# Kernel tuning notes

Hardware: AMD Instinct MI355X
Metric: run time of the kernel (lower is better)

## Reference

```python
import jax, jax.numpy as jnp
import numpy as np

B, S, D = 2, 2048, 1024
H, HKV, HD = 16, 4, 64
FF = 4096
WINDOW = 1024
EPS = 1e-6


def _rope_tables(seq_len, head_dim, base=10000.0):
    inv_freq = 1.0 / (base ** (np.arange(0, head_dim, 2, dtype=np.float32) / head_dim))
    t = np.arange(seq_len, dtype=np.float32)
    freqs = np.outer(t, inv_freq)                       # [S, HD/2]
    emb = np.concatenate([freqs, freqs], axis=-1)       # [S, HD]
    return jnp.asarray(np.cos(emb)), jnp.asarray(np.sin(emb))


def setup_inputs() -> dict:
    key = jax.random.key(0)
    ks = jax.random.split(key, 16)
    s = lambda fan: 1.0 / np.sqrt(fan)
    cos, sin = _rope_tables(S, HD)
    return {
        "hidden_states": jax.random.normal(ks[0], (B, S, D), jnp.float32),
        "cos": cos, "sin": sin,
        "wq": jax.random.normal(ks[1], (D, H * HD), jnp.float32) * s(D),
        "bq": jnp.zeros((H * HD,), jnp.float32),
        "wk": jax.random.normal(ks[2], (D, HKV * HD), jnp.float32) * s(D),
        "bk": jnp.zeros((HKV * HD,), jnp.float32),
        "wv": jax.random.normal(ks[3], (D, HKV * HD), jnp.float32) * s(D),
        "bv": jnp.zeros((HKV * HD,), jnp.float32),
        "wo": jax.random.normal(ks[4], (H * HD, D), jnp.float32) * s(H * HD),
        "ln1_w": jnp.ones((D,), jnp.float32),
        "ln2_w": jnp.ones((D,), jnp.float32),
        "w_gate": jax.random.normal(ks[5], (D, FF), jnp.float32) * s(D),
        "w_up": jax.random.normal(ks[6], (D, FF), jnp.float32) * s(D),
        "w_down": jax.random.normal(ks[7], (FF, D), jnp.float32) * s(FF),
    }


def _rmsnorm(x, w, eps=EPS):
    var = jnp.mean(x.astype(jnp.float32) ** 2, axis=-1, keepdims=True)
    return (x * jax.lax.rsqrt(var + eps)).astype(x.dtype) * w


def _rotate_half(x):
    x1, x2 = jnp.split(x, 2, axis=-1)
    return jnp.concatenate([-x2, x1], axis=-1)


def reference(hidden_states, cos, sin, wq, bq, wk, bk, wv, bv, wo,
              ln1_w, ln2_w, w_gate, w_up, w_down):
    residual = hidden_states
    h = _rmsnorm(hidden_states, ln1_w)

    # projections -> [B, S, H, HD]
    q = (h @ wq + bq).reshape(B, S, H, HD)
    k = (h @ wk + bk).reshape(B, S, HKV, HD)
    v = (h @ wv + bv).reshape(B, S, HKV, HD)

    # RoPE
    c = cos[None, :, None, :]
    sn = sin[None, :, None, :]
    q = q * c + _rotate_half(q) * sn
    k = k * c + _rotate_half(k) * sn

    # GQA: repeat KV heads to H heads
    groups = H // HKV
    k = jnp.repeat(k, groups, axis=2)  # [B, S, H, HD]
    v = jnp.repeat(v, groups, axis=2)

    # sliding-window causal attention (flex_attention block-mask semantics)
    scale = 1.0 / np.sqrt(HD)
    scores = jnp.einsum("bqhd,bkhd->bhqk", q, k) * scale  # [B, H, S, S]
    i = jnp.arange(S)[:, None]
    j = jnp.arange(S)[None, :]
    mask = (j <= i) & (i - j < WINDOW)
    scores = jnp.where(mask[None, None], scores, jnp.finfo(scores.dtype).min)
    attn = jax.nn.softmax(scores, axis=-1)
    ctx = jnp.einsum("bhqk,bkhd->bqhd", attn, v).reshape(B, S, H * HD)

    h = residual + ctx @ wo

    residual2 = h
    h2 = _rmsnorm(h, ln2_w)
    mlp = (jax.nn.silu(h2 @ w_gate) * (h2 @ w_up)) @ w_down
    return residual2 + mlp
```

## Files before the change

### kernel.cpp

```cpp
#include <hip/hip_runtime.h>
#include <hip/hip_bf16.h>
#include <hip/hip_fp16.h>
#include <math.h>

#define BB 2
#define SS 2048
#define DD 1024
#define HH 16
#define HKVN 4
#define HDIM 64
#define FFD 4096
#define WND 1024
#define EPSF 1e-6f

typedef _Float16 f16;
typedef _Float16 half8 __attribute__((ext_vector_type(8)));
typedef float f32x4 __attribute__((ext_vector_type(4)));
typedef unsigned int u32;

#define GLOAD_LDS(gp, lp)                                                  \
  __builtin_amdgcn_global_load_lds(                                        \
      (const __attribute__((address_space(1))) u32*)(gp),                  \
      (__attribute__((address_space(3))) u32*)(lp), 16, 0, 0)

static __device__ inline u32 pack2(float a, float b) {
  unsigned short ua = __builtin_bit_cast(unsigned short, (f16)a);
  unsigned short ub = __builtin_bit_cast(unsigned short, (f16)b);
  return (u32)ua | ((u32)ub << 16);
}

__global__ __launch_bounds__(256) void transpose_cast_kernel(
    const float* __restrict__ W, f16* __restrict__ Wt, int K, int N) {
  __shared__ float tile[64][65];
  int k0 = blockIdx.y * 64, n0 = blockIdx.x * 64;
  int tx = threadIdx.x & 63, tr = threadIdx.x >> 6;
#pragma unroll
  for (int i = 0; i < 16; i++) {
    int r = tr + i * 4;
    tile[r][tx] = W[(size_t)(k0 + r) * N + n0 + tx];
  }
  __syncthreads();
#pragma unroll
  for (int i = 0; i < 16; i++) {
    int r = tr + i * 4;
    Wt[(size_t)(n0 + r) * K + k0 + tx] = (f16)tile[tx][r];
  }
}

__global__ __launch_bounds__(256) void biascat_kernel(
    const float* __restrict__ bq, const float* __restrict__ bk,
    const float* __restrict__ bv, float* __restrict__ o) {
  int i = blockIdx.x * 256 + threadIdx.x;
  if (i < 1024)
    o[i] = bq[i];
  else if (i < 1280)
    o[i] = bk[i - 1024];
  else if (i < 1536)
    o[i] = bv[i - 1280];
}

__global__ __launch_bounds__(256) void rmsnorm_kernel(
    const float* __restrict__ x, const float* __restrict__ w,
    f16* __restrict__ out, int d) {
  int row = blockIdx.x;
  const float* xr = x + (size_t)row * d;
  float ss = 0.f;
  for (int i = threadIdx.x; i < d; i += blockDim.x) {
    float v = xr[i];
    ss += v * v;
  }
  __shared__ float red[8];
  for (int o = 32; o > 0; o >>= 1) ss += __shfl_down(ss, o, 64);
  int wid = threadIdx.x >> 6, lane = threadIdx.x & 63;
  if (lane == 0) red[wid] = ss;
  __syncthreads();
  if (threadIdx.x == 0) {
    float t = 0.f;
    int nw = blockDim.x >> 6;
    for (int i = 0; i < nw; i++) t += red[i];
    red[0] = rsqrtf(t / (float)d + EPSF);
  }
  __syncthreads();
  float rs = red[0];
  f16* orow = out + (size_t)row * d;
  for (int i = threadIdx.x; i < d; i += blockDim.x) {
    orow[i] = (f16)(xr[i] * rs * w[i]);
  }
}

__global__ __launch_bounds__(256) void mfma_gemm(
    const f16* __restrict__ A, const f16* __restrict__ Bt,
    const float* __restrict__ bias, const float* __restrict__ resid,
    float* __restrict__ Cf, float* __restrict__ Cf2, int M, int N, int K,
    int KL) {
  __shared__ __align__(16) char smem[3 * 16384];
  const int tid = threadIdx.x;
  const int lane = tid & 63;
  const int wid = tid >> 6;
  const int wr = wid >> 1, wc = wid & 1;
  const int row0 = blockIdx.y * 128, col0 = blockIdx.x * 128;
  const int koff = blockIdx.z * KL;

  f32x4 acc[4][4];
#pragma unroll
  for (int m = 0; m < 4; m++)
#pragma unroll
    for (int n = 0; n < 4; n++) acc[m][n] = (f32x4){0.f, 0.f, 0.f, 0.f};

  auto stage = [&](int buf, int k0) {
    char* base = smem + buf * 16384;
#pragma unroll
    for (int q = 0; q < 2; q++) {
      int s = wid * 128 + q * 64 + lane;
      int r = s >> 2;
      int cg = (s & 3) ^ ((r >> 1) & 3);
      size_t goff = (size_t)r * K + k0 + cg * 8;
      u32 ldsb = (u32)((wid * 2 + q) * 1024);
      GLOAD_LDS(A + (size_t)row0 * K + goff, base + ldsb);
      GLOAD_LDS(Bt + (size_t)col0 * K + goff, base + 8192 + ldsb);
    }
  };
  auto off = [&](int r, int g) -> int {
    return r * 64 + ((g ^ ((r >> 1) & 3)) << 4);
  };

  const int nt = KL / 32;
  stage(0, koff);
  if (nt > 1) stage(1, koff + 32);
  int cur = 0;
  const int g = lane >> 4, l15 = lane & 15;
  for (int t = 0; t < nt; t++) {
    if (t + 1 < nt)
      asm volatile("s_waitcnt vmcnt(4)" ::: "memory");
    else
      asm volatile("s_waitcnt vmcnt(0)" ::: "memory");
    asm volatile("s_waitcnt lgkmcnt(0)" ::: "memory");
    __builtin_amdgcn_sched_barrier(0);
    __builtin_amdgcn_s_barrier();
    __builtin_amdgcn_sched_barrier(0);
    const char* base = smem + cur * 16384;
    half8 af[4], bf[4];
#pragma unroll
    for (int m = 0; m < 4; m++) {
      int r = wr * 64 + m * 16 + l15;
      af[m] = *(const half8*)(base + off(r, g));
    }
#pragma unroll
    for (int n = 0; n < 4; n++) {
      int c = wc * 64 + n * 16 + l15;
      bf[n] = *(const half8*)(base + 8192 + off(c, g));
    }
    if (t + 2 < nt) {
      int nb = cur + 2;
      if (nb >= 3) nb -= 3;
      stage(nb, koff + (t + 2) * 32);
    }
    __builtin_amdgcn_s_setprio(1);
#pragma unroll
    for (int m = 0; m < 4; m++)
#pragma unroll
      for (int n = 0; n < 4; n++)
        acc[m][n] =
            __builtin_amdgcn_mfma_f32_16x16x32_f16(af[m], bf[n], acc[m][n], 0, 0, 0);
    __builtin_amdgcn_s_setprio(0);
    cur = (cur + 1 == 3) ? 0 : cur + 1;
  }

  float* cw = (blockIdx.z == 0) ? Cf : Cf2;
#pragma unroll
  for (int m = 0; m < 4; m++) {
#pragma unroll
    for (int n = 0; n < 4; n++) {
#pragma unroll
      for (int v = 0; v < 4; v++) {
        int r = row0 + wr * 64 + m * 16 + (lane >> 4) * 4 + v;
        int c = col0 + wc * 64 + n * 16 + (lane & 15);
        float vv = acc[m][n][v];
        if (bias) vv += bias[c];
        if (resid) vv += resid[(size_t)r * N + c];
        cw[(size_t)r * N + c] = vv;
      }
    }
  }
}

__global__ __launch_bounds__(512) void gateup_gemm(
    const f16* __restrict__ A, const f16* __restrict__ Wg,
    const f16* __restrict__ Wu, f16* __restrict__ ACT, int M, int N, int K) {
  __shared__ __align__(16) char smem[3 * 24576];
  const int tid = threadIdx.x;
  const int lane = tid & 63;
  const int wid = tid >> 6;
  const int wr = wid >> 1;
  const int wc = wid & 1;
  const int row0 = blockIdx.y * 128, col0 = blockIdx.x * 128;

  f32x4 accg[2][4], accu[2][4];
#pragma unroll
  for (int m = 0; m < 2; m++)
#pragma unroll
    for (int n = 0; n < 4; n++) {
      accg[m][n] = (f32x4){0.f, 0.f, 0.f, 0.f};
      accu[m][n] = (f32x4){0.f, 0.f, 0.f, 0.f};
    }

  auto stage = [&](int buf, int k0) {
    char* base = smem + buf * 24576;
    int s = tid;
    int r = s >> 2;
    int cg = (s & 3) ^ ((r >> 1) & 3);
    size_t goff = (size_t)r * K + k0 + cg * 8;
    u32 ldsb = (u32)(wid * 1024);
    GLOAD_LDS(A + (size_t)row0 * K + goff, base + ldsb);
    GLOAD_LDS(Wg + (size_t)col0 * K + goff, base + 8192 + ldsb);
    GLOAD_LDS(Wu + (size_t)col0 * K + goff, base + 16384 + ldsb);
  };
  auto off = [&](int r, int g) -> int {
    return r * 64 + ((g ^ ((r >> 1) & 3)) << 4);
  };

  const int nt = K / 32;
  stage(0, 0);
  if (nt > 1) stage(1, 32);
  int cur = 0;
  const int g = lane >> 4, l15 = lane & 15;
  for (int t = 0; t < nt; t++) {
    if (t + 1 < nt)
      asm volatile("s_waitcnt vmcnt(3)" ::: "memory");
    else
      asm volatile("s_waitcnt vmcnt(0)" ::: "memory");
    asm volatile("s_waitcnt lgkmcnt(0)" ::: "memory");
    __builtin_amdgcn_sched_barrier(0);
    __builtin_amdgcn_s_barrier();
    __builtin_amdgcn_sched_barrier(0);
    const char* base = smem + cur * 24576;
    half8 af[2], gf[4], uf[4];
#pragma unroll
    for (int m = 0; m < 2; m++) {
      int r = wr * 32 + m * 16 + l15;
      af[m] = *(const half8*)(base + off(r, g));
    }
#pragma unroll
    for (int n = 0; n < 4; n++) {
      int c = wc * 64 + n * 16 + l15;
      gf[n] = *(const half8*)(base + 8192 + off(c, g));
      uf[n] = *(const half8*)(base + 16384 + off(c, g));
    }
    if (t + 2 < nt) {
      int nb = cur + 2;
      if (nb >= 3) nb -= 3;
      stage(nb, (t + 2) * 32);
    }
    __builtin_amdgcn_s_setprio(1);
#pragma unroll
    for (int m = 0; m < 2; m++)
#pragma unroll
      for (int n = 0; n < 4; n++) {
        accg[m][n] =
            __builtin_amdgcn_mfma_f32_16x16x32_f16(af[m], gf[n], accg[m][n], 0, 0, 0);
        accu[m][n] =
            __builtin_amdgcn_mfma_f32_16x16x32_f16(af[m], uf[n], accu[m][n], 0, 0, 0);
      }
    __builtin_amdgcn_s_setprio(0);
    cur = (cur + 1 == 3) ? 0 : cur + 1;
  }

#pragma unroll
  for (int m = 0; m < 2; m++) {
#pragma unroll
    for (int n = 0; n < 4; n++) {
#pragma unroll
      for (int v = 0; v < 4; v++) {
        int r = row0 + wr * 32 + m * 16 + (lane >> 4) * 4 + v;
        int c = col0 + wc * 64 + n * 16 + (lane & 15);
        float gg = accg[m][n][v];
        float uu = accu[m][n][v];
        float sv = gg / (1.f + __expf(-gg));
        ACT[(size_t)r * N + c] = (f16)(sv * uu);
      }
    }
  }
}

__global__ __launch_bounds__(256) void addreduce_kernel(
    const float* __restrict__ P0, const float* __restrict__ P1,
    float* __restrict__ out, int n4) {
  int idx = blockIdx.x * 256 + threadIdx.x;
  for (int i = idx; i < n4; i += gridDim.x * 256) {
    float4 a = ((const float4*)P0)[i];
    float4 b = ((const float4*)P1)[i];
    float4 o = ((float4*)out)[i];
    o.x += a.x + b.x;
    o.y += a.y + b.y;
    o.z += a.z + b.z;
    o.w += a.w + b.w;
    ((float4*)out)[i] = o;
  }
}

__global__ __launch_bounds__(256) void rope_cast_kernel(
    const float* __restrict__ QKV, const float* __restrict__ cos_t,
    const float* __restrict__ sin_t, f16* __restrict__ Qh,
    f16* __restrict__ Kh) {
  int idx = blockIdx.x * blockDim.x + threadIdx.x;
  int d = idx & 31;
  int rest = idx >> 5;
  int head = rest % (HH + HKVN);
  int bs = rest / (HH + HKVN);
  int s = bs % SS;
  float c = cos_t[s * HDIM + d];
  float sn = sin_t[s * HDIM + d];
  const float* rowp = QKV + (size_t)bs * 1536;
  if (head < HH) {
    const float* base = rowp + head * HDIM;
    float x1 = base[d], x2 = base[d + 32];
    f16* ob = Qh + ((size_t)bs * HH + head) * HDIM;
    ob[d] = (f16)((x1 * c - x2 * sn) * 0.125f);
    ob[d + 32] = (f16)((x2 * c + x1 * sn) * 0.125f);
  } else {
    int hk = head - HH;
    const float* base = rowp + 1024 + hk * HDIM;
    float x1 = base[d], x2 = base[d + 32];
    f16* ob = Kh + ((size_t)bs * HKVN + hk) * HDIM;
    ob[d] = (f16)(x1 * c - x2 * sn);
    ob[d + 32] = (f16)(x2 * c + x1 * sn);
  }
}

__global__ __launch_bounds__(256) void vtrans_kernel(
    const float* __restrict__ QKV, f16* __restrict__ Vt) {
  __shared__ float tile[64][65];
  int st = blockIdx.x & 31;
  int hk = (blockIdx.x >> 5) & 3;
  int b = blockIdx.x >> 7;
  int s0 = st * 64;
  int tid = threadIdx.x;
  int r = tid >> 2, cg = tid & 3;
#pragma unroll
  for (int i = 0; i < 4; i++) {
    int c0 = cg * 16 + i * 4;
    float4 vv = *(const float4*)(QKV + (size_t)(b * SS + s0 + r) * 1536 + 1280 +
                                 hk * HDIM + c0);
    tile[r][c0 + 0] = vv.x;
    tile[r][c0 + 1] = vv.y;
    tile[r][c0 + 2] = vv.z;
    tile[r][c0 + 3] = vv.w;
  }
  __syncthreads();
  int dd = tid >> 2, sg = tid & 3;
#pragma unroll
  for (int i = 0; i < 4; i++) {
    int c0 = sg * 16 + i * 4;
    u32 w0 = pack2(tile[c0 + 0][dd], tile[c0 + 1][dd]);
    u32 w1 = pack2(tile[c0 + 2][dd], tile[c0 + 3][dd]);
    *(int2*)(Vt + ((size_t)(b * HKVN + hk) * HDIM + dd) * SS + s0 + c0) =
        make_int2((int)w0, (int)w1);
  }
}

__global__ __launch_bounds__(256) void attn_kernel(
    const f16* __restrict__ Qh, const f16* __restrict__ Kh,
    const f16* __restrict__ Vt, f16* __restrict__ O) {
  __shared__ __align__(16) char smem[2 * 16384 + 4 * 4608];
  const int tid = threadIdx.x;
  const int lane = tid & 63;
  const int wid = tid >> 6;
  const int l15 = lane & 15;
  const int g = lane >> 4;
  int qt = blockIdx.x & 63;
  int hk = (blockIdx.x >> 6) & 3;
  int b = blockIdx.x >> 8;
  int s0 = qt * 32;
  int h = hk * 4 + wid;

  half8 qf[2][2];
#pragma unroll
  for (int n = 0; n < 2; n++) {
    int q = s0 + n * 16 + l15;
    const f16* qp = Qh + (((size_t)b * SS + q) * HH + h) * HDIM;
#pragma unroll
    for (int kk = 0; kk < 2; kk++) qf[n][kk] = *(const half8*)(qp + kk * 32 + g * 8);
  }

  const int tb = (s0 >= WND) ? ((s0 - (WND - 1)) >> 6) : 0;
  const int te = (s0 + 31) >> 6;

  f32x4 acc_o[2][4];
#pragma unroll
  for (int m2 = 0; m2 < 2; m2++)
#pragma unroll
    for (int n = 0; n < 4; n++) acc_o[m2][n] = (f32x4){0.f, 0.f, 0.f, 0.f};
  float mrun[2] = {-1e30f, -1e30f};
  float lrun[2] = {0.f, 0.f};

  char* pw = smem + 32768 + wid * 4608;

  auto stage = [&](int buf, int tt) {
    int jt0 = tt * 64;
    char* kbase = smem + buf * 16384;
#pragma unroll
    for (int q2 = 0; q2 < 2; q2++) {
      int slot = (wid * 2 + q2) * 64 + lane;
      int r = slot >> 3, c = slot & 7;
      int cc = c ^ (r & 7);
      u32 ldsb = (u32)((wid * 2 + q2) * 1024);
      const f16* gk =
          Kh + ((size_t)(b * SS + jt0 + r) * HKVN + hk) * HDIM + cc * 8;
      GLOAD_LDS(gk, kbase + ldsb);
      const f16* gv =
          Vt + ((size_t)(b * HKVN + hk) * HDIM + r) * SS + jt0 + cc * 8;
      GLOAD_LDS(gv, kbase + 8192 + ldsb);
    }
  };

  stage(0, tb);
  __syncthreads();
  for (int tt = tb; tt <= te; tt++) {
    int buf = (tt - tb) & 1;
    if (tt < te) stage(buf ^ 1, tt + 1);
    const char* kb = smem + buf * 16384;
    const char* vbp = kb + 8192;
    int jt0 = tt * 64;

    f32x4 acc_s[4][2];
#pragma unroll
    for (int m = 0; m < 4; m++)
#pragma unroll
      for (int n = 0; n < 2; n++) acc_s[m][n] = (f32x4){0.f, 0.f, 0.f, 0.f};
#pragma unroll
    for (int kk = 0; kk < 2; kk++) {
      half8 af[4];
#pragma unroll
      for (int m = 0; m < 4; m++) {
        int key = m * 16 + l15;
        af[m] = *(const half8*)(kb + key * 128 + (((kk * 4 + g) ^ (key & 7)) << 4));
      }
#pragma unroll
      for (int m = 0; m < 4; m++)
#pragma unroll
        for (int n = 0; n < 2; n++)
          acc_s[m][n] = __builtin_amdgcn_mfma_f32_16x16x32_f16(af[m], qf[n][kk],
                                                               acc_s[m][n], 0, 0, 0);
    }

    float tmax[2] = {-1e38f, -1e38f};
#pragma unroll
    for (int m = 0; m < 4; m++)
#pragma unroll
      for (int n = 0; n < 2; n++)
#pragma unroll
        for (int v = 0; v < 4; v++) {
          int j = jt0 + m * 16 + g * 4 + v;
          int q = s0 + n * 16 + l15;
          float s = acc_s[m][n][v];
          s = ((unsigned)(q - j) < (unsigned)WND) ? s : -1e38f;
          acc_s[m][n][v] = s;
          tmax[n] = fmaxf(tmax[n], s);
        }
#pragma unroll
    for (int n = 0; n < 2; n++) {
      tmax[n] = fmaxf(tmax[n], __shfl_xor(tmax[n], 16, 64));
      tmax[n] = fmaxf(tmax[n], __shfl_xor(tmax[n], 32, 64));
    }
    float corr[2], rs[2];
#pragma unroll
    for (int n = 0; n < 2; n++) {
      float mn = fmaxf(mrun[n], tmax[n]);
      corr[n] = __expf(mrun[n] - mn);
      mrun[n] = mn;
      rs[n] = 0.f;
    }
#pragma unroll
    for (int m = 0; m < 4; m++)
#pragma unroll
      for (int n = 0; n < 2; n++) {
        float p0 = __expf(acc_s[m][n][0] - mrun[n]);
        float p1 = __expf(acc_s[m][n][1] - mrun[n]);
        float p2 = __expf(acc_s[m][n][2] - mrun[n]);
        float p3 = __expf(acc_s[m][n][3] - mrun[n]);
        rs[n] += (p0 + p1) + (p2 + p3);
        *(int2*)(pw + (n * 16 + l15) * 144 + (m * 16 + g * 4) * 2) =
            make_int2((int)pack2(p0, p1), (int)pack2(p2, p3));
      }
#pragma unroll
    for (int n = 0; n < 2; n++) {
      rs[n] += __shfl_xor(rs[n], 16, 64);
      rs[n] += __shfl_xor(rs[n], 32, 64);
      lrun[n] = lrun[n] * corr[n] + rs[n];
    }
#pragma unroll
    for (int m2 = 0; m2 < 2; m2++)
#pragma unroll
      for (int v = 0; v < 4; v++) {
        float cw = __shfl(corr[m2], g * 4 + v, 64);
#pragma unroll
        for (int n = 0; n < 4; n++) acc_o[m2][n][v] *= cw;
      }
#pragma unroll
    for (int kk = 0; kk < 2; kk++) {
      half8 ap[2], vf[4];
#pragma unroll
      for (int m2 = 0; m2 < 2; m2++)
        ap[m2] = *(const half8*)(pw + (m2 * 16 + l15) * 144 + (kk * 32 + g * 8) * 2);
#pragma unroll
      for (int n = 0; n < 4; n++) {
        int d = n * 16 + l15;
        vf[n] = *(const half8*)(vbp + d * 128 + (((kk * 4 + g) ^ (d & 7)) << 4));
      }
#pragma unroll
      for (int m2 = 0; m2 < 2; m2++)
#pragma unroll
        for (int n = 0; n < 4; n++)
          acc_o[m2][n] = __builtin_amdgcn_mfma_f32_16x16x32_f16(ap[m2], vf[n],
                                                                acc_o[m2][n], 0, 0, 0);
    }
    __syncthreads();
  }

#pragma unroll
  for (int m2 = 0; m2 < 2; m2++)
#pragma unroll
    for (int v = 0; v < 4; v++) {
      float li = __shfl(lrun[m2], g * 4 + v, 64);
      float inv = 1.f / li;
      int q = s0 + m2 * 16 + g * 4 + v;
#pragma unroll
      for (int n = 0; n < 4; n++) {
        int d = n * 16 + l15;
        O[(((size_t)b * SS + q) * HH + h) * HDIM + d] =
            (f16)(acc_o[m2][n][v] * inv);
      }
    }
}

extern "C" void kernel_launch(void* const* d_in, const int* in_sizes, int n_in,
                              void* d_out, int out_size, void* d_ws,
                              size_t ws_size, hipStream_t stream) {
  const float* hidden = (const float*)d_in[0];
  const float* cos_t = (const float*)d_in[1];
  const float* sin_t = (const float*)d_in[2];
  const float* wq = (const float*)d_in[3];
  const float* bq = (const float*)d_in[4];
  const float* wk = (const float*)d_in[5];
  const float* bk = (const float*)d_in[6];
  const float* wv = (const float*)d_in[7];
  const float* bv = (const float*)d_in[8];
  const float* wo = (const float*)d_in[9];
  const float* ln1 = (const float*)d_in[10];
  const float* ln2 = (const float*)d_in[11];
  const float* wg = (const float*)d_in[12];
  const float* wu = (const float*)d_in[13];
  const float* wd = (const float*)d_in[14];
  float* out = (float*)d_out;
  char* ws = (char*)d_ws;

  const int M = BB * SS;

  f16* qkvT = (f16*)ws;
  f16* woT = (f16*)(ws + (3u << 20));
  f16* wgT = (f16*)(ws + (5u << 20));
  f16* wuT = (f16*)(ws + (13u << 20));
  f16* wdT = (f16*)(ws + (21u << 20));
  f16* Anh = (f16*)(ws + (29u << 20));
  f16* CTXh = (f16*)(ws + (37u << 20));
  float* QKVb = (float*)(ws + (45u << 20));
  f16* Qh = (f16*)(ws + (69u << 20));
  f16* Kh = (f16*)(ws + (77u << 20));
  f16* Vt = (f16*)(ws + (79u << 20));
  f16* ACTh = (f16*)(ws + (45u << 20));
  float* P0 = (float*)(ws + (29u << 20));
  float* P1 = (float*)(ws + (5u << 20));
  float* biasC = (float*)(ws + (81u << 20));

  transpose_cast_kernel<<<dim3(DD / 64, DD / 64), 256, 0, stream>>>(wq, qkvT, DD, DD);
  transpose_cast_kernel<<<dim3(4, DD / 64), 256, 0, stream>>>(
      wk, qkvT + (size_t)1024 * DD, DD, 256);
  transpose_cast_kernel<<<dim3(4, DD / 64), 256, 0, stream>>>(
      wv, qkvT + (size_t)1280 * DD, DD, 256);
  transpose_cast_kernel<<<dim3(DD / 64, DD / 64), 256, 0, stream>>>(wo, woT, DD, DD);
  transpose_cast_kernel<<<dim3(FFD / 64, DD / 64), 256, 0, stream>>>(wg, wgT, DD, FFD);
  transpose_cast_kernel<<<dim3(FFD / 64, DD / 64), 256, 0, stream>>>(wu, wuT, DD, FFD);
  transpose_cast_kernel<<<dim3(DD / 64, FFD / 64), 256, 0, stream>>>(wd, wdT, FFD, DD);
  biascat_kernel<<<6, 256, 0, stream>>>(bq, bk, bv, biasC);

  rmsnorm_kernel<<<M, 256, 0, stream>>>(hidden, ln1, Anh, DD);
  mfma_gemm<<<dim3(1536 / 128, M / 128, 1), 256, 0, stream>>>(
      Anh, qkvT, biasC, nullptr, QKVb, nullptr, M, 1536, DD, DD);
  rope_cast_kernel<<<(BB * SS * (HH + HKVN) * 32) / 256, 256, 0, stream>>>(
      QKVb, cos_t, sin_t, Qh, Kh);
  vtrans_kernel<<<BB * HKVN * (SS / 64), 256, 0, stream>>>(QKVb, Vt);
  attn_kernel<<<BB * HKVN * (SS / 32), 256, 0, stream>>>(Qh, Kh, Vt, CTXh);
  mfma_gemm<<<dim3(DD / 128, M / 128, 1), 256, 0, stream>>>(
      CTXh, woT, nullptr, hidden, out, nullptr, M, DD, DD, DD);
  rmsnorm_kernel<<<M, 256, 0, stream>>>(out, ln2, Anh, DD);
  gateup_gemm<<<dim3(FFD / 128, M / 128), 512, 0, stream>>>(Anh, wgT, wuT, ACTh,
                                                            M, FFD, DD);
  mfma_gemm<<<dim3(DD / 128, M / 128, 2), 256, 0, stream>>>(
      ACTh, wdT, nullptr, nullptr, P0, P1, M, DD, FFD, FFD / 2);
  addreduce_kernel<<<2048, 256, 0, stream>>>(P0, P1, out, M * DD / 4);
}
```

Measured before the change: 295.7 us.

## Enlarge GEMM tiles to 256 rows/cols and emit QKV projection in fp16

```diff
diff --git a/kernel.cpp b/kernel.cpp
--- a/kernel.cpp
+++ b/kernel.cpp
@@ -88,36 +88,43 @@
   }
 }
 
-__global__ __launch_bounds__(256) void mfma_gemm(
+__global__ __launch_bounds__(256) void gemm_ww(
     const f16* __restrict__ A, const f16* __restrict__ Bt,
     const float* __restrict__ bias, const float* __restrict__ resid,
-    float* __restrict__ Cf, float* __restrict__ Cf2, int M, int N, int K,
-    int KL) {
-  __shared__ __align__(16) char smem[3 * 16384];
+    float* __restrict__ Cf, float* __restrict__ Cf2, f16* __restrict__ Ch,
+    int M, int N, int K, int KL) {
+  __shared__ __align__(16) char smem[3 * 24576];
   const int tid = threadIdx.x;
   const int lane = tid & 63;
   const int wid = tid >> 6;
   const int wr = wid >> 1, wc = wid & 1;
-  const int row0 = blockIdx.y * 128, col0 = blockIdx.x * 128;
+  const int row0 = blockIdx.y * 256, col0 = blockIdx.x * 128;
   const int koff = blockIdx.z * KL;
 
-  f32x4 acc[4][4];
-#pragma unroll
-  for (int m = 0; m < 4; m++)
+  f32x4 acc[8][4];
+#pragma unroll
+  for (int m = 0; m < 8; m++)
 #pragma unroll
     for (int n = 0; n < 4; n++) acc[m][n] = (f32x4){0.f, 0.f, 0.f, 0.f};
 
   auto stage = [&](int buf, int k0) {
-    char* base = smem + buf * 16384;
-#pragma unroll
-    for (int q = 0; q < 2; q++) {
-      int s = wid * 128 + q * 64 + lane;
+    char* base = smem + buf * 24576;
+#pragma unroll
+    for (int p = 0; p < 4; p++) {
+      int s = p * 256 + tid;
       int r = s >> 2;
       int cg = (s & 3) ^ ((r >> 1) & 3);
       size_t goff = (size_t)r * K + k0 + cg * 8;
-      u32 ldsb = (u32)((wid * 2 + q) * 1024);
-      GLOAD_LDS(A + (size_t)row0 * K + goff, base + ldsb);
-      GLOAD_LDS(Bt + (size_t)col0 * K + goff, base + 8192 + ldsb);
+      GLOAD_LDS(A + (size_t)row0 * K + goff, base + p * 4096 + wid * 1024);
+    }
+#pragma unroll
+    for (int p = 0; p < 2; p++) {
+      int s = p * 256 + tid;
+      int r = s >> 2;
+      int cg = (s & 3) ^ ((r >> 1) & 3);
+      size_t goff = (size_t)r * K + k0 + cg * 8;
+      GLOAD_LDS(Bt + (size_t)col0 * K + goff,
+                base + 16384 + p * 4096 + wid * 1024);
     }
   };
   auto off = [&](int r, int g) -> int {
@@ -131,24 +138,24 @@
   const int g = lane >> 4, l15 = lane & 15;
   for (int t = 0; t < nt; t++) {
     if (t + 1 < nt)
-      asm volatile("s_waitcnt vmcnt(4)" ::: "memory");
+      asm volatile("s_waitcnt vmcnt(6)" ::: "memory");
     else
       asm volatile("s_waitcnt vmcnt(0)" ::: "memory");
     asm volatile("s_waitcnt lgkmcnt(0)" ::: "memory");
     __builtin_amdgcn_sched_barrier(0);
     __builtin_amdgcn_s_barrier();
     __builtin_amdgcn_sched_barrier(0);
-    const char* base = smem + cur * 16384;
-    half8 af[4], bf[4];
-#pragma unroll
-    for (int m = 0; m < 4; m++) {
-      int r = wr * 64 + m * 16 + l15;
+    const char* base = smem + cur * 24576;
+    half8 af[8], bf[4];
+#pragma unroll
+    for (int m = 0; m < 8; m++) {
+      int r = wr * 128 + m * 16 + l15;
       af[m] = *(const half8*)(base + off(r, g));
     }
 #pragma unroll
     for (int n = 0; n < 4; n++) {
       int c = wc * 64 + n * 16 + l15;
-      bf[n] = *(const half8*)(base + 8192 + off(c, g));
+      bf[n] = *(const half8*)(base + 16384 + off(c, g));
     }
     if (t + 2 < nt) {
       int nb = cur + 2;
@@ -157,7 +164,7 @@
     }
     __builtin_amdgcn_s_setprio(1);
 #pragma unroll
-    for (int m = 0; m < 4; m++)
+    for (int m = 0; m < 8; m++)
 #pragma unroll
       for (int n = 0; n < 4; n++)
         acc[m][n] =
@@ -168,17 +175,21 @@
 
   float* cw = (blockIdx.z == 0) ? Cf : Cf2;
 #pragma unroll
-  for (int m = 0; m < 4; m++) {
+  for (int m = 0; m < 8; m++) {
 #pragma unroll
     for (int n = 0; n < 4; n++) {
 #pragma unroll
       for (int v = 0; v < 4; v++) {
-        int r = row0 + wr * 64 + m * 16 + (lane >> 4) * 4 + v;
-        int c = col0 + wc * 64 + n * 16 + (lane & 15);
+        int r = row0 + wr * 128 + m * 16 + (lane >> 4) * 4 + v;
+        int c = col0 + wc * 64 + n * 16 + l15;
         float vv = acc[m][n][v];
         if (bias) vv += bias[c];
-        if (resid) vv += resid[(size_t)r * N + c];
-        cw[(size_t)r * N + c] = vv;
+        if (Ch) {
+          Ch[(size_t)r * N + c] = (f16)vv;
+        } else {
+          if (resid) vv += resid[(size_t)r * N + c];
+          cw[(size_t)r * N + c] = vv;
+        }
       }
     }
   }
@@ -187,17 +198,17 @@
 __global__ __launch_bounds__(512) void gateup_gemm(
     const f16* __restrict__ A, const f16* __restrict__ Wg,
     const f16* __restrict__ Wu, f16* __restrict__ ACT, int M, int N, int K) {
-  __shared__ __align__(16) char smem[3 * 24576];
+  __shared__ __align__(16) char smem[3 * 40960];
   const int tid = threadIdx.x;
   const int lane = tid & 63;
   const int wid = tid >> 6;
-  const int wr = wid >> 1;
-  const int wc = wid & 1;
-  const int row0 = blockIdx.y * 128, col0 = blockIdx.x * 128;
-
-  f32x4 accg[2][4], accu[2][4];
-#pragma unroll
-  for (int m = 0; m < 2; m++)
+  const int wr = wid >> 2;
+  const int wc = wid & 3;
+  const int row0 = blockIdx.y * 128, col0 = blockIdx.x * 256;
+
+  f32x4 accg[4][4], accu[4][4];
+#pragma unroll
+  for (int m = 0; m < 4; m++)
 #pragma unroll
     for (int n = 0; n < 4; n++) {
       accg[m][n] = (f32x4){0.f, 0.f, 0.f, 0.f};
@@ -205,15 +216,32 @@
     }
 
   auto stage = [&](int buf, int k0) {
-    char* base = smem + buf * 24576;
-    int s = tid;
-    int r = s >> 2;
-    int cg = (s & 3) ^ ((r >> 1) & 3);
-    size_t goff = (size_t)r * K + k0 + cg * 8;
-    u32 ldsb = (u32)(wid * 1024);
-    GLOAD_LDS(A + (size_t)row0 * K + goff, base + ldsb);
-    GLOAD_LDS(Wg + (size_t)col0 * K + goff, base + 8192 + ldsb);
-    GLOAD_LDS(Wu + (size_t)col0 * K + goff, base + 16384 + ldsb);
+    char* base = smem + buf * 40960;
+    {
+      int s = tid;
+      int r = s >> 2;
+      int cg = (s & 3) ^ ((r >> 1) & 3);
+      size_t goff = (size_t)r * K + k0 + cg * 8;
+      GLOAD_LDS(A + (size_t)row0 * K + goff, base + wid * 1024);
+    }
+#pragma unroll
+    for (int p = 0; p < 2; p++) {
+      int s = p * 512 + tid;
+      int r = s >> 2;
+      int cg = (s & 3) ^ ((r >> 1) & 3);
+      size_t goff = (size_t)r * K + k0 + cg * 8;
+      GLOAD_LDS(Wg + (size_t)col0 * K + goff,
+                base + 8192 + p * 8192 + wid * 1024);
+    }
+#pragma unroll
+    for (int p = 0; p < 2; p++) {
+      int s = p * 512 + tid;
+      int r = s >> 2;
+      int cg = (s & 3) ^ ((r >> 1) & 3);
+      size_t goff = (size_t)r * K + k0 + cg * 8;
+      GLOAD_LDS(Wu + (size_t)col0 * K + goff,
+                base + 24576 + p * 8192 + wid * 1024);
+    }
   };
   auto off = [&](int r, int g) -> int {
     return r * 64 + ((g ^ ((r >> 1) & 3)) << 4);
@@ -226,25 +254,25 @@
   const int g = lane >> 4, l15 = lane & 15;
   for (int t = 0; t < nt; t++) {
     if (t + 1 < nt)
-      asm volatile("s_waitcnt vmcnt(3)" ::: "memory");
+      asm volatile("s_waitcnt vmcnt(5)" ::: "memory");
     else
       asm volatile("s_waitcnt vmcnt(0)" ::: "memory");
     asm volatile("s_waitcnt lgkmcnt(0)" ::: "memory");
     __builtin_amdgcn_sched_barrier(0);
     __builtin_amdgcn_s_barrier();
     __builtin_amdgcn_sched_barrier(0);
-    const char* base = smem + cur * 24576;
-    half8 af[2], gf[4], uf[4];
-#pragma unroll
-    for (int m = 0; m < 2; m++) {
-      int r = wr * 32 + m * 16 + l15;
+    const char* base = smem + cur * 40960;
+    half8 af[4], gf[4], uf[4];
+#pragma unroll
+    for (int m = 0; m < 4; m++) {
+      int r = wr * 64 + m * 16 + l15;
       af[m] = *(const half8*)(base + off(r, g));
     }
 #pragma unroll
     for (int n = 0; n < 4; n++) {
       int c = wc * 64 + n * 16 + l15;
       gf[n] = *(const half8*)(base + 8192 + off(c, g));
-      uf[n] = *(const half8*)(base + 16384 + off(c, g));
+      uf[n] = *(const half8*)(base + 24576 + off(c, g));
     }
     if (t + 2 < nt) {
       int nb = cur + 2;
@@ -253,7 +281,7 @@
     }
     __builtin_amdgcn_s_setprio(1);
 #pragma unroll
-    for (int m = 0; m < 2; m++)
+    for (int m = 0; m < 4; m++)
 #pragma unroll
       for (int n = 0; n < 4; n++) {
         accg[m][n] =
@@ -266,13 +294,13 @@
   }
 
 #pragma unroll
-  for (int m = 0; m < 2; m++) {
+  for (int m = 0; m < 4; m++) {
 #pragma unroll
     for (int n = 0; n < 4; n++) {
 #pragma unroll
       for (int v = 0; v < 4; v++) {
-        int r = row0 + wr * 32 + m * 16 + (lane >> 4) * 4 + v;
-        int c = col0 + wc * 64 + n * 16 + (lane & 15);
+        int r = row0 + wr * 64 + m * 16 + (lane >> 4) * 4 + v;
+        int c = col0 + wc * 64 + n * 16 + l15;
         float gg = accg[m][n][v];
         float uu = accu[m][n][v];
         float sv = gg / (1.f + __expf(-gg));
@@ -299,7 +327,7 @@
 }
 
 __global__ __launch_bounds__(256) void rope_cast_kernel(
-    const float* __restrict__ QKV, const float* __restrict__ cos_t,
+    const f16* __restrict__ QKV, const float* __restrict__ cos_t,
     const float* __restrict__ sin_t, f16* __restrict__ Qh,
     f16* __restrict__ Kh) {
   int idx = blockIdx.x * blockDim.x + threadIdx.x;
@@ -310,17 +338,17 @@
   int s = bs % SS;
   float c = cos_t[s * HDIM + d];
   float sn = sin_t[s * HDIM + d];
-  const float* rowp = QKV + (size_t)bs * 1536;
+  const f16* rowp = QKV + (size_t)bs * 1536;
   if (head < HH) {
-    const float* base = rowp + head * HDIM;
-    float x1 = base[d], x2 = base[d + 32];
+    const f16* base = rowp + head * HDIM;
+    float x1 = (float)base[d], x2 = (float)base[d + 32];
     f16* ob = Qh + ((size_t)bs * HH + head) * HDIM;
     ob[d] = (f16)((x1 * c - x2 * sn) * 0.125f);
     ob[d + 32] = (f16)((x2 * c + x1 * sn) * 0.125f);
   } else {
     int hk = head - HH;
-    const float* base = rowp + 1024 + hk * HDIM;
-    float x1 = base[d], x2 = base[d + 32];
+    const f16* base = rowp + 1024 + hk * HDIM;
+    float x1 = (float)base[d], x2 = (float)base[d + 32];
     f16* ob = Kh + ((size_t)bs * HKVN + hk) * HDIM;
     ob[d] = (f16)(x1 * c - x2 * sn);
     ob[d + 32] = (f16)(x2 * c + x1 * sn);
@@ -328,8 +356,8 @@
 }
 
 __global__ __launch_bounds__(256) void vtrans_kernel(
-    const float* __restrict__ QKV, f16* __restrict__ Vt) {
-  __shared__ float tile[64][65];
+    const f16* __restrict__ QKV, f16* __restrict__ Vt) {
+  __shared__ f16 tile[64][72];
   int st = blockIdx.x & 31;
   int hk = (blockIdx.x >> 5) & 3;
   int b = blockIdx.x >> 7;
@@ -337,22 +365,22 @@
   int tid = threadIdx.x;
   int r = tid >> 2, cg = tid & 3;
 #pragma unroll
-  for (int i = 0; i < 4; i++) {
-    int c0 = cg * 16 + i * 4;
-    float4 vv = *(const float4*)(QKV + (size_t)(b * SS + s0 + r) * 1536 + 1280 +
-                                 hk * HDIM + c0);
-    tile[r][c0 + 0] = vv.x;
-    tile[r][c0 + 1] = vv.y;
-    tile[r][c0 + 2] = vv.z;
-    tile[r][c0 + 3] = vv.w;
+  for (int i = 0; i < 2; i++) {
+    const f16* src = QKV + (size_t)(b * SS + s0 + r) * 1536 + 1280 + hk * HDIM +
+                     cg * 16 + i * 8;
+    *(int4*)&tile[r][cg * 16 + i * 8] = *(const int4*)src;
   }
   __syncthreads();
   int dd = tid >> 2, sg = tid & 3;
 #pragma unroll
   for (int i = 0; i < 4; i++) {
     int c0 = sg * 16 + i * 4;
-    u32 w0 = pack2(tile[c0 + 0][dd], tile[c0 + 1][dd]);
-    u32 w1 = pack2(tile[c0 + 2][dd], tile[c0 + 3][dd]);
+    unsigned short a0 = __builtin_bit_cast(unsigned short, tile[c0 + 0][dd]);
+    unsigned short a1 = __builtin_bit_cast(unsigned short, tile[c0 + 1][dd]);
+    unsigned short a2 = __builtin_bit_cast(unsigned short, tile[c0 + 2][dd]);
+    unsigned short a3 = __builtin_bit_cast(unsigned short, tile[c0 + 3][dd]);
+    u32 w0 = (u32)a0 | ((u32)a1 << 16);
+    u32 w1 = (u32)a2 | ((u32)a3 << 16);
     *(int2*)(Vt + ((size_t)(b * HKVN + hk) * HDIM + dd) * SS + s0 + c0) =
         make_int2((int)w0, (int)w1);
   }
@@ -563,10 +591,10 @@
   f16* wdT = (f16*)(ws + (21u << 20));
   f16* Anh = (f16*)(ws + (29u << 20));
   f16* CTXh = (f16*)(ws + (37u << 20));
-  float* QKVb = (float*)(ws + (45u << 20));
-  f16* Qh = (f16*)(ws + (69u << 20));
-  f16* Kh = (f16*)(ws + (77u << 20));
-  f16* Vt = (f16*)(ws + (79u << 20));
+  f16* QKVh = (f16*)(ws + (45u << 20));
+  f16* Qh = (f16*)(ws + (57u << 20));
+  f16* Kh = (f16*)(ws + (65u << 20));
+  f16* Vt = (f16*)(ws + (67u << 20));
   f16* ACTh = (f16*)(ws + (45u << 20));
   float* P0 = (float*)(ws + (29u << 20));
   float* P1 = (float*)(ws + (5u << 20));
@@ -584,18 +612,18 @@
   biascat_kernel<<<6, 256, 0, stream>>>(bq, bk, bv, biasC);
 
   rmsnorm_kernel<<<M, 256, 0, stream>>>(hidden, ln1, Anh, DD);
-  mfma_gemm<<<dim3(1536 / 128, M / 128, 1), 256, 0, stream>>>(
-      Anh, qkvT, biasC, nullptr, QKVb, nullptr, M, 1536, DD, DD);
+  gemm_ww<<<dim3(1536 / 128, M / 256, 1), 256, 0, stream>>>(
+      Anh, qkvT, biasC, nullptr, nullptr, nullptr, QKVh, M, 1536, DD, DD);
   rope_cast_kernel<<<(BB * SS * (HH + HKVN) * 32) / 256, 256, 0, stream>>>(
-      QKVb, cos_t, sin_t, Qh, Kh);
-  vtrans_kernel<<<BB * HKVN * (SS / 64), 256, 0, stream>>>(QKVb, Vt);
+      QKVh, cos_t, sin_t, Qh, Kh);
+  vtrans_kernel<<<BB * HKVN * (SS / 64), 256, 0, stream>>>(QKVh, Vt);
   attn_kernel<<<BB * HKVN * (SS / 32), 256, 0, stream>>>(Qh, Kh, Vt, CTXh);
-  mfma_gemm<<<dim3(DD / 128, M / 128, 1), 256, 0, stream>>>(
-      CTXh, woT, nullptr, hidden, out, nullptr, M, DD, DD, DD);
+  gemm_ww<<<dim3(DD / 128, M / 256, 1), 256, 0, stream>>>(
+      CTXh, woT, nullptr, hidden, out, nullptr, nullptr, M, DD, DD, DD);
   rmsnorm_kernel<<<M, 256, 0, stream>>>(out, ln2, Anh, DD);
-  gateup_gemm<<<dim3(FFD / 128, M / 128), 512, 0, stream>>>(Anh, wgT, wuT, ACTh,
+  gateup_gemm<<<dim3(FFD / 256, M / 128), 512, 0, stream>>>(Anh, wgT, wuT, ACTh,
                                                             M, FFD, DD);
-  mfma_gemm<<<dim3(DD / 128, M / 128, 2), 256, 0, stream>>>(
-      ACTh, wdT, nullptr, nullptr, P0, P1, M, DD, FFD, FFD / 2);
+  gemm_ww<<<dim3(DD / 128, M / 256, 2), 256, 0, stream>>>(
+      ACTh, wdT, nullptr, nullptr, P0, P1, nullptr, M, DD, FFD, FFD / 2);
   addreduce_kernel<<<2048, 256, 0, stream>>>(P0, P1, out, M * DD / 4);
 }
```

After: 319.3 us. 8.0% more time.
